# Kernel optimization log

Hardware: AMD Instinct MI355X
Metric: run time of the kernel (lower is better)

Reference implementation:

```python
import jax, jax.numpy as jnp
import numpy as np

TOKENS, IN_DIM = 4096, 4096
N_EXPERTS, OUT_DIM = 8, 14336


def setup_inputs() -> dict:
    key = jax.random.key(0)
    k1, k2 = jax.random.split(key)
    state = jax.random.normal(k1, (TOKENS, IN_DIM), dtype=jnp.float32)
    # stacked per-expert weights, stored [n_experts, out_dim, in_dim] as in vLLM
    w = jax.random.normal(k2, (N_EXPERTS, OUT_DIM, IN_DIM), dtype=jnp.float32) * 0.02
    expert_id = 3
    return {"state": state, "w": w, "expert_id": expert_id}


def reference(state, w, expert_id):
    # w[expert_id] : [out_dim, in_dim]; transpose(0,1) -> [in_dim, out_dim]
    # state @ weight : [tokens, out_dim]
    weight = w[expert_id]  # gather one expert's matrix
    return jnp.einsum('ti,oi->to', state, weight)
```

## Files before the change

kernel.cpp:

```cpp
#include <hip/hip_runtime.h>
#include <hip/hip_bf16.h>

#define M_TOK 4096
#define K_DIM 4096
#define N_OUT 14336
#define NT (K_DIM / 64)

typedef float f32x4 __attribute__((ext_vector_type(4)));
typedef short bf16x8 __attribute__((ext_vector_type(8)));
typedef unsigned short u16;
typedef unsigned int u32;
typedef u16 u16x8 __attribute__((ext_vector_type(8)));

__device__ __forceinline__ u16 f2bf_rne(float f) {
    u32 u = __builtin_bit_cast(u32, f);
    u += 0x7fffu + ((u >> 16) & 1u);
    return (u16)(u >> 16);
}

__device__ __forceinline__ void async16(const void* g, void* l) {
    __builtin_amdgcn_global_load_lds(
        (const __attribute__((address_space(1))) void*)g,
        (__attribute__((address_space(3))) void*)l, 16, 0, 0);
}

__device__ __forceinline__ void bar() {
    asm volatile("" ::: "memory");
    __builtin_amdgcn_s_barrier();
    asm volatile("" ::: "memory");
}

#define VMCNT(n) asm volatile("s_waitcnt vmcnt(" #n ")" ::: "memory")


__global__ __launch_bounds__(256) void cvt_state_kernel(const float* __restrict__ src,
                                                        u16* __restrict__ dst) {
    size_t i = ((size_t)blockIdx.x * 256 + threadIdx.x) * 8;
    f32x4 v0 = *(const f32x4*)(src + i);
    f32x4 v1 = *(const f32x4*)(src + i + 4);
    u16x8 h;
    h[0] = f2bf_rne(v0[0]); h[1] = f2bf_rne(v0[1]);
    h[2] = f2bf_rne(v0[2]); h[3] = f2bf_rne(v0[3]);
    h[4] = f2bf_rne(v1[0]); h[5] = f2bf_rne(v1[1]);
    h[6] = f2bf_rne(v1[2]); h[7] = f2bf_rne(v1[3]);
    *(u16x8*)(dst + i) = h;
}

__global__ __launch_bounds__(256) void cvt_w_kernel(const float* __restrict__ w,
                                                    const int* __restrict__ eid,
                                                    u16* __restrict__ dst) {
    const float* src = w + (size_t)(*eid) * ((size_t)N_OUT * K_DIM);
    size_t i = ((size_t)blockIdx.x * 256 + threadIdx.x) * 8;
    f32x4 v0 = *(const f32x4*)(src + i);
    f32x4 v1 = *(const f32x4*)(src + i + 4);
    u16x8 h;
    h[0] = f2bf_rne(v0[0]); h[1] = f2bf_rne(v0[1]);
    h[2] = f2bf_rne(v0[2]); h[3] = f2bf_rne(v0[3]);
    h[4] = f2bf_rne(v1[0]); h[5] = f2bf_rne(v1[1]);
    h[6] = f2bf_rne(v1[2]); h[7] = f2bf_rne(v1[3]);
    *(u16x8*)(dst + i) = h;
}


__global__ __launch_bounds__(512, 2) void gemm256_8p(const u16* __restrict__ A,
                                                     const u16* __restrict__ B,
                                                     float* __restrict__ C) {
    __shared__ __align__(16) u16 lds[2][2][16384];

    const int tid  = threadIdx.x;
    const int wid  = tid >> 6;
    const int lane = tid & 63;
    const int wr = wid >> 2;
    const int wc = wid & 3;
    const int brow = blockIdx.y * 256;
    const int bcol = blockIdx.x * 256;

    const int rsel = lane >> 3;
    const int slot = lane & 7;
    const int scol = ((slot ^ rsel) << 3);
    u32 aoff[2][2], boff[2][2];
#pragma unroll
    for (int h = 0; h < 2; ++h)
#pragma unroll
        for (int c = 0; c < 2; ++c) {
            const int row = h * 128 + wid * 8 + c * 64 + rsel;
            aoff[h][c] = (u32)(brow + row) * K_DIM + scol;
            boff[h][c] = (u32)(bcol + row) * K_DIM + scol;
        }

    const int la = lane & 15, kb = lane >> 4, l7 = lane & 7;
    const int aB[2] = {(wr * 128 + la) * 64 + ((kb ^ l7) << 3),
                       (wr * 128 + la) * 64 + (((4 + kb) ^ l7) << 3)};
    const int bB[2] = {(wc * 64 + la) * 64 + ((kb ^ l7) << 3),
                       (wc * 64 + la) * 64 + (((4 + kb) ^ l7) << 3)};

    f32x4 acc[8][4] = {};
    bf16x8 aF0[4][2], aF1[4][2], bF[2][2];

#define STAGE_A(buf, h, kt) do { \
    async16(A + aoff[h][0] + (u32)(kt) * 64, &lds[buf][0][(h) * 8192 + wid * 512]); \
    async16(A + aoff[h][1] + (u32)(kt) * 64, &lds[buf][0][(h) * 8192 + wid * 512 + 4096]); \
} while (0)
#define STAGE_B(buf, h, kt) do { \
    async16(B + boff[h][0] + (u32)(kt) * 64, &lds[buf][1][(h) * 8192 + wid * 512]); \
    async16(B + boff[h][1] + (u32)(kt) * 64, &lds[buf][1][(h) * 8192 + wid * 512 + 4096]); \
} while (0)

#define LD_A0(buf) do { \
    _Pragma("unroll") for (int m = 0; m < 4; ++m) \
    _Pragma("unroll") for (int ks = 0; ks < 2; ++ks) \
        aF0[m][ks] = *(const bf16x8*)&lds[buf][0][aB[ks] + m * 1024]; \
} while (0)
#define LD_A1(buf) do { \
    _Pragma("unroll") for (int m = 0; m < 4; ++m) \
    _Pragma("unroll") for (int ks = 0; ks < 2; ++ks) \
        aF1[m][ks] = *(const bf16x8*)&lds[buf][0][aB[ks] + (m + 4) * 1024]; \
} while (0)
#define LD_B01(buf) do { \
    _Pragma("unroll") for (int n = 0; n < 2; ++n) \
    _Pragma("unroll") for (int ks = 0; ks < 2; ++ks) \
        bF[n][ks] = *(const bf16x8*)&lds[buf][1][bB[ks] + n * 1024]; \
} while (0)
#define LD_B23(buf) do { \
    _Pragma("unroll") for (int n = 0; n < 2; ++n) \
    _Pragma("unroll") for (int ks = 0; ks < 2; ++ks) \
        bF[n][ks] = *(const bf16x8*)&lds[buf][1][bB[ks] + (n + 2) * 1024]; \
} while (0)

#define MMQ(AA, QM, QN) do { \
    __builtin_amdgcn_s_setprio(1); \
    _Pragma("unroll") for (int m = 0; m < 4; ++m) \
    _Pragma("unroll") for (int n = 0; n < 2; ++n) \
    _Pragma("unroll") for (int ks = 0; ks < 2; ++ks) \
        acc[(QM) * 4 + m][(QN) * 2 + n] = __builtin_amdgcn_mfma_f32_16x16x32_bf16( \
            AA[m][ks], bF[n][ks], acc[(QM) * 4 + m][(QN) * 2 + n], 0, 0, 0); \
    __builtin_amdgcn_s_setprio(0); \
} while (0)

    STAGE_A(0, 0, 0); STAGE_A(0, 1, 0); STAGE_B(0, 0, 0); STAGE_B(0, 1, 0);
    STAGE_A(1, 0, 1);
    STAGE_A(1, 1, 1); STAGE_B(1, 0, 1);
    VMCNT(6);
    __builtin_amdgcn_s_barrier();
    asm volatile("" ::: "memory");

#pragma unroll 1
    for (int it = 0; it < NT / 2; ++it) {
        const int t1 = 2 * it + 1;
        const int t2 = (2 * it + 2) & (NT - 1);
        const int t3 = (2 * it + 3) & (NT - 1);
        LD_A0(0); LD_B01(0);
        STAGE_B(1, 1, t1);
        bar(); MMQ(aF0, 0, 0); bar();
        LD_A1(0);
        bar(); MMQ(aF1, 1, 0); bar();
        LD_B23(0);
        STAGE_A(0, 0, t2);
        bar(); MMQ(aF0, 0, 1); bar();
        STAGE_A(0, 1, t2); STAGE_B(0, 0, t2);
        bar(); MMQ(aF1, 1, 1);
        VMCNT(6); bar();
        LD_A0(1); LD_B01(1);
        STAGE_B(0, 1, t2);
        bar(); MMQ(aF0, 0, 0); bar();
        LD_A1(1);
        bar(); MMQ(aF1, 1, 0); bar();
        LD_B23(1);
        STAGE_A(1, 0, t3);
        bar(); MMQ(aF0, 0, 1); bar();
        STAGE_A(1, 1, t3); STAGE_B(1, 0, t3);
        bar(); MMQ(aF1, 1, 1);
        VMCNT(6); bar();
    }

    asm volatile("" ::: "memory");
#pragma unroll
    for (int mi = 0; mi < 8; ++mi)
#pragma unroll
        for (int n = 0; n < 4; ++n) {
            float* cp = C + (size_t)(brow + wr * 128 + mi * 16 + kb * 4) * N_OUT
                          + (bcol + wc * 64 + n * 16 + la);
#pragma unroll
            for (int j = 0; j < 4; ++j)
                cp[(size_t)j * N_OUT] = acc[mi][n][j];
        }
}


__global__ __launch_bounds__(256) void gemm_fused(const float* __restrict__ Af,
                                                  const float* __restrict__ Wf,
                                                  const int* __restrict__ eid,
                                                  float* __restrict__ C) {
    const float* Bf = Wf + (size_t)(*eid) * ((size_t)N_OUT * K_DIM);

    __shared__ __align__(16) u16 As[2][4096];
    __shared__ __align__(16) u16 Bs[2][4096];

    const int tid  = threadIdx.x;
    const int wid  = tid >> 6;
    const int lane = tid & 63;
    const int brow = blockIdx.y * 128;
    const int bcol = blockIdx.x * 128;
    const int wr = wid >> 1, wc = wid & 1;

    f32x4 acc[4][4] = {};

    auto stage = [&](int buf, int kt) {
#pragma unroll
        for (int i = 0; i < 2; ++i) {
            const int l = tid + i * 256;
            const int g = l >> 6, c4 = (l >> 4) & 3, r = l & 15;
            {
                const size_t base = (size_t)(brow + g * 16 + r) * K_DIM + c4 * 8 + kt * 32;
                f32x4 v0 = *(const f32x4*)(Af + base);
                f32x4 v1 = *(const f32x4*)(Af + base + 4);
                u16x8 h;
                h[0] = f2bf_rne(v0[0]); h[1] = f2bf_rne(v0[1]);
                h[2] = f2bf_rne(v0[2]); h[3] = f2bf_rne(v0[3]);
                h[4] = f2bf_rne(v1[0]); h[5] = f2bf_rne(v1[1]);
                h[6] = f2bf_rne(v1[2]); h[7] = f2bf_rne(v1[3]);
                *(u16x8*)&As[buf][l * 8] = h;
            }
            {
                const size_t base = (size_t)(bcol + g * 16 + r) * K_DIM + c4 * 8 + kt * 32;
                f32x4 v0 = *(const f32x4*)(Bf + base);
                f32x4 v1 = *(const f32x4*)(Bf + base + 4);
                u16x8 h;
                h[0] = f2bf_rne(v0[0]); h[1] = f2bf_rne(v0[1]);
                h[2] = f2bf_rne(v0[2]); h[3] = f2bf_rne(v0[3]);
                h[4] = f2bf_rne(v1[0]); h[5] = f2bf_rne(v1[1]);
                h[6] = f2bf_rne(v1[2]); h[7] = f2bf_rne(v1[3]);
                *(u16x8*)&Bs[buf][l * 8] = h;
            }
        }
    };

    auto compute = [&](int buf) {
        bf16x8 a[4], b[4];
#pragma unroll
        for (int m = 0; m < 4; ++m)
            a[m] = *(const bf16x8*)&As[buf][(wr * 4 + m) * 512 + lane * 8];
#pragma unroll
        for (int n = 0; n < 4; ++n)
            b[n] = *(const bf16x8*)&Bs[buf][(wc * 4 + n) * 512 + lane * 8];
#pragma unroll
        for (int m = 0; m < 4; ++m)
#pragma unroll
            for (int n = 0; n < 4; ++n)
                acc[m][n] = __builtin_amdgcn_mfma_f32_16x16x32_bf16(a[m], b[n], acc[m][n], 0, 0, 0);
    };

    stage(0, 0);
    __syncthreads();
    int cur = 0;
#pragma unroll 1
    for (int kt = 0; kt < (K_DIM / 32) - 1; ++kt) {
        stage(cur ^ 1, kt + 1);
        compute(cur);
        __syncthreads();
        cur ^= 1;
    }
    compute(cur);

    const int r0 = (lane >> 4) * 4;
    const int cn = lane & 15;
#pragma unroll
    for (int m = 0; m < 4; ++m)
#pragma unroll
        for (int n = 0; n < 4; ++n) {
            float* cp = C + (size_t)(brow + wr * 64 + m * 16 + r0) * N_OUT
                          + (bcol + wc * 64 + n * 16 + cn);
#pragma unroll
            for (int j = 0; j < 4; ++j)
                cp[(size_t)j * N_OUT] = acc[m][n][j];
        }
}


extern "C" void kernel_launch(void* const* d_in, const int* in_sizes, int n_in,
                              void* d_out, int out_size, void* d_ws, size_t ws_size,
                              hipStream_t stream) {
    const float* state = (const float*)d_in[0];
    const float* w     = (const float*)d_in[1];
    const int*   eid   = (const int*)d_in[2];
    float*       out   = (float*)d_out;

    const size_t nA = (size_t)M_TOK * K_DIM;
    const size_t nB = (size_t)N_OUT * K_DIM;
    const size_t need = (nA + nB) * sizeof(u16);

    if (d_ws != nullptr && ws_size >= need) {
        u16* a16 = (u16*)d_ws;
        u16* b16 = a16 + nA;
        cvt_state_kernel<<<(unsigned)(nA / 2048), 256, 0, stream>>>(state, a16);
        cvt_w_kernel<<<(unsigned)(nB / 2048), 256, 0, stream>>>(w, eid, b16);
        dim3 grid(N_OUT / 256, M_TOK / 256);
        gemm256_8p<<<grid, 512, 0, stream>>>(a16, b16, out);
    } else {
        dim3 grid(N_OUT / 128, M_TOK / 128);
        gemm_fused<<<grid, 256, 0, stream>>>(state, w, eid, out);
    }
}
```

Before: 503.2 us.

## Split GEMM into full-wave main pass plus half-tile tail, fuse conversion kernels

Merges the two fp32-to-bf16 conversion kernels into one launch. The main 256x256 GEMM now runs only 768 of the 896 tiles, assigned through an XCD-aware remapping of the block index. The remaining 128 tiles are split into 256 half-width (256x128) blocks handled by a new tail kernel with triple-buffered A, which evens out wave quantization on the last wave. It also inserts an lgkmcnt wait hint before the MFMA phases, at the cost of an extra kernel launch and more code.

```diff
diff --git a/kernel.cpp b/kernel.cpp
--- a/kernel.cpp
+++ b/kernel.cpp
@@ -31,34 +31,34 @@
 }
 
 #define VMCNT(n) asm volatile("s_waitcnt vmcnt(" #n ")" ::: "memory")
-
-
-__global__ __launch_bounds__(256) void cvt_state_kernel(const float* __restrict__ src,
-                                                        u16* __restrict__ dst) {
-    size_t i = ((size_t)blockIdx.x * 256 + threadIdx.x) * 8;
-    f32x4 v0 = *(const f32x4*)(src + i);
-    f32x4 v1 = *(const f32x4*)(src + i + 4);
+#define LGKM_HINT() asm volatile("s_waitcnt lgkmcnt(8)" ::: "memory")
+
+
+__global__ __launch_bounds__(256) void cvt_all(const float* __restrict__ state,
+                                               const float* __restrict__ w,
+                                               const int* __restrict__ eid,
+                                               u16* __restrict__ a16,
+                                               u16* __restrict__ b16) {
+    const size_t nA = (size_t)M_TOK * K_DIM;
+    size_t base = (size_t)blockIdx.x * 2048 + (size_t)threadIdx.x * 8;
+    const float* src;
+    u16* dst;
+    if (base < nA) {
+        src = state + base;
+        dst = a16 + base;
+    } else {
+        size_t j = base - nA;
+        src = w + (size_t)(*eid) * ((size_t)N_OUT * K_DIM) + j;
+        dst = b16 + j;
+    }
+    f32x4 v0 = *(const f32x4*)(src);
+    f32x4 v1 = *(const f32x4*)(src + 4);
     u16x8 h;
     h[0] = f2bf_rne(v0[0]); h[1] = f2bf_rne(v0[1]);
     h[2] = f2bf_rne(v0[2]); h[3] = f2bf_rne(v0[3]);
     h[4] = f2bf_rne(v1[0]); h[5] = f2bf_rne(v1[1]);
     h[6] = f2bf_rne(v1[2]); h[7] = f2bf_rne(v1[3]);
-    *(u16x8*)(dst + i) = h;
-}
-
-__global__ __launch_bounds__(256) void cvt_w_kernel(const float* __restrict__ w,
-                                                    const int* __restrict__ eid,
-                                                    u16* __restrict__ dst) {
-    const float* src = w + (size_t)(*eid) * ((size_t)N_OUT * K_DIM);
-    size_t i = ((size_t)blockIdx.x * 256 + threadIdx.x) * 8;
-    f32x4 v0 = *(const f32x4*)(src + i);
-    f32x4 v1 = *(const f32x4*)(src + i + 4);
-    u16x8 h;
-    h[0] = f2bf_rne(v0[0]); h[1] = f2bf_rne(v0[1]);
-    h[2] = f2bf_rne(v0[2]); h[3] = f2bf_rne(v0[3]);
-    h[4] = f2bf_rne(v1[0]); h[5] = f2bf_rne(v1[1]);
-    h[6] = f2bf_rne(v1[2]); h[7] = f2bf_rne(v1[3]);
-    *(u16x8*)(dst + i) = h;
+    *(u16x8*)(dst) = h;
 }
 
 
@@ -66,14 +66,19 @@
                                                      const u16* __restrict__ B,
                                                      float* __restrict__ C) {
     __shared__ __align__(16) u16 lds[2][2][16384];
+
+    const int bid  = blockIdx.x;
+    const int tile = (bid & 7) * 96 + (bid >> 3);
+    const int by   = tile / 56;
+    const int bx   = tile % 56;
+    const int brow = by * 256;
+    const int bcol = bx * 256;
 
     const int tid  = threadIdx.x;
     const int wid  = tid >> 6;
     const int lane = tid & 63;
     const int wr = wid >> 2;
     const int wc = wid & 3;
-    const int brow = blockIdx.y * 256;
-    const int bcol = blockIdx.x * 256;
 
     const int rsel = lane >> 3;
     const int slot = lane & 7;
@@ -151,6 +156,7 @@
         const int t3 = (2 * it + 3) & (NT - 1);
         LD_A0(0); LD_B01(0);
         STAGE_B(1, 1, t1);
+        LGKM_HINT();
         bar(); MMQ(aF0, 0, 0); bar();
         LD_A1(0);
         bar(); MMQ(aF1, 1, 0); bar();
@@ -162,6 +168,7 @@
         VMCNT(6); bar();
         LD_A0(1); LD_B01(1);
         STAGE_B(0, 1, t2);
+        LGKM_HINT();
         bar(); MMQ(aF0, 0, 0); bar();
         LD_A1(1);
         bar(); MMQ(aF1, 1, 0); bar();
@@ -180,6 +187,136 @@
         for (int n = 0; n < 4; ++n) {
             float* cp = C + (size_t)(brow + wr * 128 + mi * 16 + kb * 4) * N_OUT
                           + (bcol + wc * 64 + n * 16 + la);
+#pragma unroll
+            for (int j = 0; j < 4; ++j)
+                cp[(size_t)j * N_OUT] = acc[mi][n][j];
+        }
+}
+
+
+__global__ __launch_bounds__(512, 2) void gemm256_tail(const u16* __restrict__ A,
+                                                       const u16* __restrict__ B,
+                                                       float* __restrict__ C) {
+    __shared__ __align__(16) u16 ldsA[3][16384];
+    __shared__ __align__(16) u16 ldsB[2][8192];
+
+    const int bid  = blockIdx.x;
+    const int tb   = (bid & 7) * 32 + (bid >> 3);
+    const int tile = 768 + (tb >> 1);
+    const int half = tb & 1;
+    const int by   = tile / 56;
+    const int bx   = tile % 56;
+    const int brow = by * 256;
+    const int bcol = bx * 256 + half * 128;
+
+    const int tid  = threadIdx.x;
+    const int wid  = tid >> 6;
+    const int lane = tid & 63;
+    const int wr = wid >> 2;
+    const int wc = wid & 3;
+
+    const int rsel = lane >> 3;
+    const int slot = lane & 7;
+    const int scol = ((slot ^ rsel) << 3);
+    u32 aoff[2][2], boff[2];
+#pragma unroll
+    for (int h = 0; h < 2; ++h)
+#pragma unroll
+        for (int c = 0; c < 2; ++c) {
+            const int row = h * 128 + wid * 8 + c * 64 + rsel;
+            aoff[h][c] = (u32)(brow + row) * K_DIM + scol;
+        }
+#pragma unroll
+    for (int c = 0; c < 2; ++c) {
+        const int row = wid * 8 + c * 64 + rsel;
+        boff[c] = (u32)(bcol + row) * K_DIM + scol;
+    }
+
+    const int la = lane & 15, kb = lane >> 4, l7 = lane & 7;
+    const int aB[2] = {(wr * 128 + la) * 64 + ((kb ^ l7) << 3),
+                       (wr * 128 + la) * 64 + (((4 + kb) ^ l7) << 3)};
+    const int bB[2] = {(wc * 32 + la) * 64 + ((kb ^ l7) << 3),
+                       (wc * 32 + la) * 64 + (((4 + kb) ^ l7) << 3)};
+
+    f32x4 acc[8][2] = {};
+    bf16x8 aF0[4][2], aF1[4][2], bF[2][2];
+
+#define T_STAGE_A(ab, h, kt) do { \
+    async16(A + aoff[h][0] + (u32)(kt) * 64, &ldsA[ab][(h) * 8192 + wid * 512]); \
+    async16(A + aoff[h][1] + (u32)(kt) * 64, &ldsA[ab][(h) * 8192 + wid * 512 + 4096]); \
+} while (0)
+#define T_STAGE_B(bb, kt) do { \
+    async16(B + boff[0] + (u32)(kt) * 64, &ldsB[bb][wid * 512]); \
+    async16(B + boff[1] + (u32)(kt) * 64, &ldsB[bb][wid * 512 + 4096]); \
+} while (0)
+
+#define T_LD_A0(ab) do { \
+    _Pragma("unroll") for (int m = 0; m < 4; ++m) \
+    _Pragma("unroll") for (int ks = 0; ks < 2; ++ks) \
+        aF0[m][ks] = *(const bf16x8*)&ldsA[ab][aB[ks] + m * 1024]; \
+} while (0)
+#define T_LD_A1(ab) do { \
+    _Pragma("unroll") for (int m = 0; m < 4; ++m) \
+    _Pragma("unroll") for (int ks = 0; ks < 2; ++ks) \
+        aF1[m][ks] = *(const bf16x8*)&ldsA[ab][aB[ks] + (m + 4) * 1024]; \
+} while (0)
+#define T_LD_B(bb) do { \
+    _Pragma("unroll") for (int n = 0; n < 2; ++n) \
+    _Pragma("unroll") for (int ks = 0; ks < 2; ++ks) \
+        bF[n][ks] = *(const bf16x8*)&ldsB[bb][bB[ks] + n * 1024]; \
+} while (0)
+
+#define MMQ_T(AA, QM) do { \
+    __builtin_amdgcn_s_setprio(1); \
+    _Pragma("unroll") for (int m = 0; m < 4; ++m) \
+    _Pragma("unroll") for (int n = 0; n < 2; ++n) \
+    _Pragma("unroll") for (int ks = 0; ks < 2; ++ks) \
+        acc[(QM) * 4 + m][n] = __builtin_amdgcn_mfma_f32_16x16x32_bf16( \
+            AA[m][ks], bF[n][ks], acc[(QM) * 4 + m][n], 0, 0, 0); \
+    __builtin_amdgcn_s_setprio(0); \
+} while (0)
+
+    T_STAGE_A(0, 0, 0); T_STAGE_A(0, 1, 0); T_STAGE_B(0, 0);
+    T_STAGE_A(1, 0, 1); T_STAGE_A(1, 1, 1); T_STAGE_B(1, 1);
+    VMCNT(6);
+    __builtin_amdgcn_s_barrier();
+    asm volatile("" ::: "memory");
+
+#pragma unroll 1
+    for (int it = 0; it < NT / 2; ++it) {
+        const int t  = 2 * it;
+        const int t2 = (t + 2) & (NT - 1);
+        const int t3 = (t + 3) & (NT - 1);
+        const int a0 = t % 3;
+        const int a1 = (a0 + 1) % 3;
+        const int a2 = (a0 + 2) % 3;
+        T_LD_A0(a0); T_LD_B(0);
+        T_STAGE_A(a2, 0, t2);
+        LGKM_HINT();
+        bar(); MMQ_T(aF0, 0); bar();
+        T_LD_A1(a0);
+        T_STAGE_A(a2, 1, t2);
+        bar(); MMQ_T(aF1, 1);
+        VMCNT(4); bar();
+        T_LD_A0(a1); T_LD_B(1);
+        T_STAGE_B(0, t2);
+        T_STAGE_A(a0, 0, t3);
+        LGKM_HINT();
+        bar(); MMQ_T(aF0, 0); bar();
+        T_LD_A1(a1);
+        T_STAGE_A(a0, 1, t3);
+        T_STAGE_B(1, t3);
+        bar(); MMQ_T(aF1, 1);
+        VMCNT(6); bar();
+    }
+
+    asm volatile("" ::: "memory");
+#pragma unroll
+    for (int mi = 0; mi < 8; ++mi)
+#pragma unroll
+        for (int n = 0; n < 2; ++n) {
+            float* cp = C + (size_t)(brow + wr * 128 + mi * 16 + kb * 4) * N_OUT
+                          + (bcol + wc * 32 + n * 16 + la);
 #pragma unroll
             for (int j = 0; j < 4; ++j)
                 cp[(size_t)j * N_OUT] = acc[mi][n][j];
@@ -292,10 +429,9 @@
     if (d_ws != nullptr && ws_size >= need) {
         u16* a16 = (u16*)d_ws;
         u16* b16 = a16 + nA;
-        cvt_state_kernel<<<(unsigned)(nA / 2048), 256, 0, stream>>>(state, a16);
-        cvt_w_kernel<<<(unsigned)(nB / 2048), 256, 0, stream>>>(w, eid, b16);
-        dim3 grid(N_OUT / 256, M_TOK / 256);
-        gemm256_8p<<<grid, 512, 0, stream>>>(a16, b16, out);
+        cvt_all<<<(unsigned)((nA + nB) / 2048), 256, 0, stream>>>(state, w, eid, a16, b16);
+        gemm256_8p<<<768, 512, 0, stream>>>(a16, b16, out);
+        gemm256_tail<<<256, 512, 0, stream>>>(a16, b16, out);
     } else {
         dim3 grid(N_OUT / 128, M_TOK / 128);
         gemm_fused<<<grid, 256, 0, stream>>>(state, w, eid, out);
```

After: 523.0 us. +3.9%, slower.

## Split-K the tail wave of GEMM tiles and merge conversion kernels

Applied to the files above, without the earlier changes.

Merges the two fp32-to-bf16 conversion kernels into one launch. Splits the 896 output tiles into a 768-tile main GEMM and a last 128 tiles computed as split-K halves (256 blocks), with the second half written to a workspace and added back by a reduction kernel. The aim is to shrink the partially filled final wave on the 256-CU device. It costs two extra launches, extra workspace traffic and a read-modify-write of the tail output, and it only takes this path when the workspace is large enough.

```diff
diff --git a/kernel.cpp b/kernel.cpp
--- a/kernel.cpp
+++ b/kernel.cpp
@@ -4,7 +4,6 @@
 #define M_TOK 4096
 #define K_DIM 4096
 #define N_OUT 14336
-#define NT (K_DIM / 64)
 
 typedef float f32x4 __attribute__((ext_vector_type(4)));
 typedef short bf16x8 __attribute__((ext_vector_type(8)));
@@ -33,47 +32,46 @@
 #define VMCNT(n) asm volatile("s_waitcnt vmcnt(" #n ")" ::: "memory")
 
 
-__global__ __launch_bounds__(256) void cvt_state_kernel(const float* __restrict__ src,
-                                                        u16* __restrict__ dst) {
-    size_t i = ((size_t)blockIdx.x * 256 + threadIdx.x) * 8;
-    f32x4 v0 = *(const f32x4*)(src + i);
-    f32x4 v1 = *(const f32x4*)(src + i + 4);
+__global__ __launch_bounds__(256) void cvt_all(const float* __restrict__ state,
+                                               const float* __restrict__ w,
+                                               const int* __restrict__ eid,
+                                               u16* __restrict__ a16,
+                                               u16* __restrict__ b16) {
+    const size_t nA = (size_t)M_TOK * K_DIM;
+    size_t base = (size_t)blockIdx.x * 2048 + (size_t)threadIdx.x * 8;
+    const float* src;
+    u16* dst;
+    if (base < nA) {
+        src = state + base;
+        dst = a16 + base;
+    } else {
+        size_t j = base - nA;
+        src = w + (size_t)(*eid) * ((size_t)N_OUT * K_DIM) + j;
+        dst = b16 + j;
+    }
+    f32x4 v0 = *(const f32x4*)(src);
+    f32x4 v1 = *(const f32x4*)(src + 4);
     u16x8 h;
     h[0] = f2bf_rne(v0[0]); h[1] = f2bf_rne(v0[1]);
     h[2] = f2bf_rne(v0[2]); h[3] = f2bf_rne(v0[3]);
     h[4] = f2bf_rne(v1[0]); h[5] = f2bf_rne(v1[1]);
     h[6] = f2bf_rne(v1[2]); h[7] = f2bf_rne(v1[3]);
-    *(u16x8*)(dst + i) = h;
-}
-
-__global__ __launch_bounds__(256) void cvt_w_kernel(const float* __restrict__ w,
-                                                    const int* __restrict__ eid,
-                                                    u16* __restrict__ dst) {
-    const float* src = w + (size_t)(*eid) * ((size_t)N_OUT * K_DIM);
-    size_t i = ((size_t)blockIdx.x * 256 + threadIdx.x) * 8;
-    f32x4 v0 = *(const f32x4*)(src + i);
-    f32x4 v1 = *(const f32x4*)(src + i + 4);
-    u16x8 h;
-    h[0] = f2bf_rne(v0[0]); h[1] = f2bf_rne(v0[1]);
-    h[2] = f2bf_rne(v0[2]); h[3] = f2bf_rne(v0[3]);
-    h[4] = f2bf_rne(v1[0]); h[5] = f2bf_rne(v1[1]);
-    h[6] = f2bf_rne(v1[2]); h[7] = f2bf_rne(v1[3]);
-    *(u16x8*)(dst + i) = h;
-}
-
-
-__global__ __launch_bounds__(512, 2) void gemm256_8p(const u16* __restrict__ A,
-                                                     const u16* __restrict__ B,
-                                                     float* __restrict__ C) {
-    __shared__ __align__(16) u16 lds[2][2][16384];
-
+    *(u16x8*)(dst) = h;
+}
+
+
+template <int NKT>
+__device__ __forceinline__ void gemm_body(const u16* __restrict__ A,
+                                          const u16* __restrict__ B,
+                                          float* __restrict__ out, int ldc,
+                                          int orow, int ocol,
+                                          int brow, int bcol, int k0t,
+                                          u16* ldsb) {
     const int tid  = threadIdx.x;
     const int wid  = tid >> 6;
     const int lane = tid & 63;
     const int wr = wid >> 2;
     const int wc = wid & 3;
-    const int brow = blockIdx.y * 256;
-    const int bcol = blockIdx.x * 256;
 
     const int rsel = lane >> 3;
     const int slot = lane & 7;
@@ -84,8 +82,8 @@
 #pragma unroll
         for (int c = 0; c < 2; ++c) {
             const int row = h * 128 + wid * 8 + c * 64 + rsel;
-            aoff[h][c] = (u32)(brow + row) * K_DIM + scol;
-            boff[h][c] = (u32)(bcol + row) * K_DIM + scol;
+            aoff[h][c] = (u32)(brow + row) * K_DIM + scol + (u32)k0t * 64;
+            boff[h][c] = (u32)(bcol + row) * K_DIM + scol + (u32)k0t * 64;
         }
 
     const int la = lane & 15, kb = lane >> 4, l7 = lane & 7;
@@ -98,33 +96,33 @@
     bf16x8 aF0[4][2], aF1[4][2], bF[2][2];
 
 #define STAGE_A(buf, h, kt) do { \
-    async16(A + aoff[h][0] + (u32)(kt) * 64, &lds[buf][0][(h) * 8192 + wid * 512]); \
-    async16(A + aoff[h][1] + (u32)(kt) * 64, &lds[buf][0][(h) * 8192 + wid * 512 + 4096]); \
+    async16(A + aoff[h][0] + (u32)(kt) * 64, ldsb + (buf) * 32768 + (h) * 8192 + wid * 512); \
+    async16(A + aoff[h][1] + (u32)(kt) * 64, ldsb + (buf) * 32768 + (h) * 8192 + wid * 512 + 4096); \
 } while (0)
 #define STAGE_B(buf, h, kt) do { \
-    async16(B + boff[h][0] + (u32)(kt) * 64, &lds[buf][1][(h) * 8192 + wid * 512]); \
-    async16(B + boff[h][1] + (u32)(kt) * 64, &lds[buf][1][(h) * 8192 + wid * 512 + 4096]); \
+    async16(B + boff[h][0] + (u32)(kt) * 64, ldsb + (buf) * 32768 + 16384 + (h) * 8192 + wid * 512); \
+    async16(B + boff[h][1] + (u32)(kt) * 64, ldsb + (buf) * 32768 + 16384 + (h) * 8192 + wid * 512 + 4096); \
 } while (0)
 
 #define LD_A0(buf) do { \
     _Pragma("unroll") for (int m = 0; m < 4; ++m) \
     _Pragma("unroll") for (int ks = 0; ks < 2; ++ks) \
-        aF0[m][ks] = *(const bf16x8*)&lds[buf][0][aB[ks] + m * 1024]; \
+        aF0[m][ks] = *(const bf16x8*)&ldsb[(buf) * 32768 + aB[ks] + m * 1024]; \
 } while (0)
 #define LD_A1(buf) do { \
     _Pragma("unroll") for (int m = 0; m < 4; ++m) \
     _Pragma("unroll") for (int ks = 0; ks < 2; ++ks) \
-        aF1[m][ks] = *(const bf16x8*)&lds[buf][0][aB[ks] + (m + 4) * 1024]; \
+        aF1[m][ks] = *(const bf16x8*)&ldsb[(buf) * 32768 + aB[ks] + (m + 4) * 1024]; \
 } while (0)
 #define LD_B01(buf) do { \
     _Pragma("unroll") for (int n = 0; n < 2; ++n) \
     _Pragma("unroll") for (int ks = 0; ks < 2; ++ks) \
-        bF[n][ks] = *(const bf16x8*)&lds[buf][1][bB[ks] + n * 1024]; \
+        bF[n][ks] = *(const bf16x8*)&ldsb[(buf) * 32768 + 16384 + bB[ks] + n * 1024]; \
 } while (0)
 #define LD_B23(buf) do { \
     _Pragma("unroll") for (int n = 0; n < 2; ++n) \
     _Pragma("unroll") for (int ks = 0; ks < 2; ++ks) \
-        bF[n][ks] = *(const bf16x8*)&lds[buf][1][bB[ks] + (n + 2) * 1024]; \
+        bF[n][ks] = *(const bf16x8*)&ldsb[(buf) * 32768 + 16384 + bB[ks] + (n + 2) * 1024]; \
 } while (0)
 
 #define MMQ(AA, QM, QN) do { \
@@ -145,10 +143,10 @@
     asm volatile("" ::: "memory");
 
 #pragma unroll 1
-    for (int it = 0; it < NT / 2; ++it) {
+    for (int it = 0; it < NKT / 2; ++it) {
         const int t1 = 2 * it + 1;
-        const int t2 = (2 * it + 2) & (NT - 1);
-        const int t3 = (2 * it + 3) & (NT - 1);
+        const int t2 = (2 * it + 2) & (NKT - 1);
+        const int t3 = (2 * it + 3) & (NKT - 1);
         LD_A0(0); LD_B01(0);
         STAGE_B(1, 1, t1);
         bar(); MMQ(aF0, 0, 0); bar();
@@ -178,12 +176,71 @@
     for (int mi = 0; mi < 8; ++mi)
 #pragma unroll
         for (int n = 0; n < 4; ++n) {
-            float* cp = C + (size_t)(brow + wr * 128 + mi * 16 + kb * 4) * N_OUT
-                          + (bcol + wc * 64 + n * 16 + la);
+            float* cp = out + (size_t)(orow + wr * 128 + mi * 16 + kb * 4) * (size_t)ldc
+                            + (ocol + wc * 64 + n * 16 + la);
 #pragma unroll
             for (int j = 0; j < 4; ++j)
-                cp[(size_t)j * N_OUT] = acc[mi][n][j];
+                cp[(size_t)j * ldc] = acc[mi][n][j];
         }
+
+#undef STAGE_A
+#undef STAGE_B
+#undef LD_A0
+#undef LD_A1
+#undef LD_B01
+#undef LD_B23
+#undef MMQ
+}
+
+__global__ __launch_bounds__(512, 2) void gemm256_main(const u16* __restrict__ A,
+                                                       const u16* __restrict__ B,
+                                                       float* __restrict__ C) {
+    __shared__ __align__(16) u16 lds[2][2][16384];
+    const int tile = blockIdx.x;
+    const int by = tile / 56, bx = tile % 56;
+    gemm_body<64>(A, B, C, N_OUT, by * 256, bx * 256, by * 256, bx * 256, 0,
+                  &lds[0][0][0]);
+}
+
+__global__ __launch_bounds__(512, 2) void gemm256_tailk(const u16* __restrict__ A,
+                                                        const u16* __restrict__ B,
+                                                        float* __restrict__ C,
+                                                        float* __restrict__ ws) {
+    __shared__ __align__(16) u16 lds[2][2][16384];
+    const int bid = blockIdx.x;
+    const int tb = bid & 127;
+    const int kh = bid >> 7;
+    const int tile = 768 + tb;
+    const int by = tile / 56, bx = tile % 56;
+    if (kh == 0) {
+        gemm_body<32>(A, B, C, N_OUT, by * 256, bx * 256, by * 256, bx * 256, 0,
+                      &lds[0][0][0]);
+    } else {
+        gemm_body<32>(A, B, ws + (size_t)tb * 65536, 256, 0, 0,
+                      by * 256, bx * 256, 32, &lds[0][0][0]);
+    }
+}
+
+__global__ __launch_bounds__(256) void reduce_tail(const float* __restrict__ ws,
+                                                   float* __restrict__ C) {
+    const int bid = blockIdx.x;
+    const int tb = bid >> 4;
+    const int rg = bid & 15;
+    const int tile = 768 + tb;
+    const int by = tile / 56, bx = tile % 56;
+    const float* src = ws + (size_t)tb * 65536 + rg * 4096;
+    float* dst = C + (size_t)(by * 256 + rg * 16) * N_OUT + bx * 256;
+    const int tidx = threadIdx.x;
+#pragma unroll
+    for (int p = 0; p < 4; ++p) {
+        const int e = p * 1024 + tidx * 4;
+        const int r = e >> 8, c = e & 255;
+        f32x4 v = *(const f32x4*)(src + e);
+        float* d = dst + (size_t)r * N_OUT + c;
+        f32x4 o = *(const f32x4*)d;
+        o[0] += v[0]; o[1] += v[1]; o[2] += v[2]; o[3] += v[3];
+        *(f32x4*)d = o;
+    }
 }
 
 
@@ -287,15 +344,22 @@
 
     const size_t nA = (size_t)M_TOK * K_DIM;
     const size_t nB = (size_t)N_OUT * K_DIM;
-    const size_t need = (nA + nB) * sizeof(u16);
-
-    if (d_ws != nullptr && ws_size >= need) {
+    const size_t needA = (nA + nB) * sizeof(u16);
+    const size_t needB = needA + (size_t)128 * 65536 * 4;
+
+    if (d_ws != nullptr && ws_size >= needB) {
         u16* a16 = (u16*)d_ws;
         u16* b16 = a16 + nA;
-        cvt_state_kernel<<<(unsigned)(nA / 2048), 256, 0, stream>>>(state, a16);
-        cvt_w_kernel<<<(unsigned)(nB / 2048), 256, 0, stream>>>(w, eid, b16);
-        dim3 grid(N_OUT / 256, M_TOK / 256);
-        gemm256_8p<<<grid, 512, 0, stream>>>(a16, b16, out);
+        float* wsC = (float*)((char*)d_ws + needA);
+        cvt_all<<<(unsigned)((nA + nB) / 2048), 256, 0, stream>>>(state, w, eid, a16, b16);
+        gemm256_main<<<768, 512, 0, stream>>>(a16, b16, out);
+        gemm256_tailk<<<256, 512, 0, stream>>>(a16, b16, out, wsC);
+        reduce_tail<<<2048, 256, 0, stream>>>(wsC, out);
+    } else if (d_ws != nullptr && ws_size >= needA) {
+        u16* a16 = (u16*)d_ws;
+        u16* b16 = a16 + nA;
+        cvt_all<<<(unsigned)((nA + nB) / 2048), 256, 0, stream>>>(state, w, eid, a16, b16);
+        gemm256_main<<<896, 512, 0, stream>>>(a16, b16, out);
     } else {
         dim3 grid(N_OUT / 128, M_TOK / 128);
         gemm_fused<<<grid, 256, 0, stream>>>(state, w, eid, out);
```

Measured after the change: 489.4 us. 1.03x faster.
